# Performance work log

Measured on AMD Instinct MI355X. Metric: run time of the kernel, lower is better.

The kernel has to match this reference:

```python
import jax, jax.numpy as jnp
import numpy as np

N = 8192
IN_FEATS = 512
OUT_FEATS = 512


def setup_inputs() -> dict:
    key = jax.random.key(0)
    k_adj, k_feat, k_w = jax.random.split(key, 3)
    adj = jax.random.uniform(k_adj, (N, N), dtype=jnp.float32)
    features = jax.random.normal(k_feat, (N, IN_FEATS), dtype=jnp.float32)
    # nn.Linear(in_feats, out_feats, bias=False): weight is [out, in]; we store transposed [in, out]
    W = jax.random.normal(k_w, (IN_FEATS, OUT_FEATS), dtype=jnp.float32) / np.sqrt(IN_FEATS)
    return {"adj": adj, "features": features, "W": W}


def reference(adj, features, W):
    n = adj.shape[0]
    # adj + I (self loops)
    a = adj + jnp.eye(n, dtype=adj.dtype)
    # symmetric degree normalization D^{-1/2} A D^{-1/2}
    deg = jnp.sum(a, axis=1)  # [N]
    d_inv_sqrt = jnp.where(deg > 0, jax.lax.rsqrt(deg), 0.0)  # inf -> 0 as in torch code
    # diag(d) @ a @ diag(d) == d[:,None] * a * d[None,:] (algebraic simplification of O(N^3) diag matmuls)
    norm_adj = d_inv_sqrt[:, None] * a * d_inv_sqrt[None, :]  # [N, N]
    h = norm_adj @ features  # [N, in]
    return h @ W  # [N, out]
```

## Files before the change

### kernel.cpp

```cpp
#include <hip/hip_runtime.h>
#include <cstdint>
#include <cstddef>

#define NN 8192
#define NF 512
#define SPLITK 4

typedef __attribute__((ext_vector_type(8))) short bf16x8;
typedef __attribute__((ext_vector_type(8))) unsigned short u16x8;
typedef __attribute__((ext_vector_type(4))) float f32x4;

__device__ __forceinline__ unsigned short f2bf_bits(float f) {
  unsigned u = __builtin_bit_cast(unsigned, f);
  u += 0x7FFFu + ((u >> 16) & 1u);
  return (unsigned short)(u >> 16);
}

__device__ __forceinline__ float bf2f(unsigned short b) {
  return __builtin_bit_cast(float, (unsigned)b << 16);
}

__device__ __forceinline__ bf16x8 cvt8(float4 a, float4 b) {
  bf16x8 r;
  r[0] = (short)f2bf_bits(a.x); r[1] = (short)f2bf_bits(a.y);
  r[2] = (short)f2bf_bits(a.z); r[3] = (short)f2bf_bits(a.w);
  r[4] = (short)f2bf_bits(b.x); r[5] = (short)f2bf_bits(b.y);
  r[6] = (short)f2bf_bits(b.z); r[7] = (short)f2bf_bits(b.w);
  return r;
}

__device__ __forceinline__ void gld_lds16(const void* g, void* l) {
  __builtin_amdgcn_global_load_lds(
      (const __attribute__((address_space(1))) unsigned int*)g,
      (__attribute__((address_space(3))) unsigned int*)l, 16, 0, 0);
}

template <bool CVT>
__global__ void k_rowsum(const float* __restrict__ adj, float* __restrict__ dinv,
                         short* __restrict__ adjb) {
  const int row = blockIdx.x;
  const float4* p = (const float4*)(adj + (size_t)row * NN);
  short* ob = CVT ? (adjb + (size_t)row * NN) : nullptr;
  float s = 0.f;
#pragma unroll
  for (int j = 0; j < 8; ++j) {
    float4 v = p[j * 256 + threadIdx.x];
    s += (v.x + v.y) + (v.z + v.w);
    if (CVT) {
      ushort4 o;
      o.x = f2bf_bits(v.x); o.y = f2bf_bits(v.y);
      o.z = f2bf_bits(v.z); o.w = f2bf_bits(v.w);
      *(ushort4*)&ob[(size_t)(j * 256 + threadIdx.x) * 4] = o;
    }
  }
#pragma unroll
  for (int off = 32; off > 0; off >>= 1) s += __shfl_down(s, off, 64);
  __shared__ float red[4];
  if ((threadIdx.x & 63) == 0) red[threadIdx.x >> 6] = s;
  __syncthreads();
  if (threadIdx.x == 0) {
    float deg = red[0] + red[1] + red[2] + red[3] + 1.0f;
    dinv[row] = (deg > 0.f) ? (1.0f / sqrtf(deg)) : 0.f;
  }
}

__global__ void k_transpose2(const float* __restrict__ feat, const float* __restrict__ W,
                             const float* __restrict__ dinv,
                             short* __restrict__ FbT, short* __restrict__ WbT) {
  __shared__ float tile[32][33];
  const bool isF = (blockIdx.y < (NN / 32));
  const float* src = isF ? feat : W;
  short* dst = isF ? FbT : WbT;
  const int rows = isF ? NN : NF;
  const int r0 = (isF ? blockIdx.y : (blockIdx.y - NN / 32)) * 32;
  const int c0 = blockIdx.x * 32;
  const int tx = threadIdx.x & 31, ty = threadIdx.x >> 5;
#pragma unroll
  for (int i = 0; i < 32; i += 8) {
    float v = src[(size_t)(r0 + ty + i) * NF + c0 + tx];
    if (isF) v *= dinv[r0 + ty + i];
    tile[ty + i][tx] = v;
  }
  __syncthreads();
#pragma unroll
  for (int i = 0; i < 32; i += 8)
    dst[(size_t)(c0 + ty + i) * rows + r0 + tx] = (short)f2bf_bits(tile[tx][ty + i]);
}

__global__ __launch_bounds__(512, 1)
void k_gemm8(const short* __restrict__ Ab, const short* __restrict__ Bt,
             int N, int K, unsigned short* __restrict__ Pout) {
  __shared__ __align__(16) short As[3][2][256 * 32];
  __shared__ __align__(16) short Bs[2][2][256 * 32];
  const int tid = threadIdx.x, lane = tid & 63, w = tid >> 6;
  const int wm = w >> 2, wn = w & 3;

  const int hid = (blockIdx.z * gridDim.y + blockIdx.y) * gridDim.x + blockIdx.x;
  const int xcd = hid & 7, rr = hid >> 3;
  const int pair = xcd * 16 + (rr >> 1);
  const int member = rr & 1;
  const int m0 = (pair & 31) * 256;
  const int n0 = member * 256;
  const int kz = pair >> 5;
  const int ksl = K / SPLITK;
  const int kbase = kz * ksl;
  const int nt = ksl >> 6;
  unsigned short* Cp = Pout + (size_t)kz * ((size_t)NN * (size_t)N);

  f32x4 acc[8][4];
#pragma unroll
  for (int m = 0; m < 8; ++m)
#pragma unroll
    for (int n = 0; n < 4; ++n) acc[m][n] = (f32x4){0.f, 0.f, 0.f, 0.f};

  const int lr = lane & 15, kg = lane >> 4;

  auto stageA = [&](int buf, int t) {
#pragma unroll
    for (int h = 0; h < 2; ++h) {
      const int kofs = kbase + (t << 6) + (h << 5) + ((lane & 3) << 3);
#pragma unroll
      for (int rnd = 0; rnd < 2; ++rnd) {
        const int rowb = (rnd << 7) + (w << 4);
        const int row = rowb + (lane >> 2);
        gld_lds16(Ab + (size_t)(m0 + row) * K + kofs, &As[buf][h][rowb << 5]);
      }
    }
  };
  auto stageB = [&](int buf, int t) {
#pragma unroll
    for (int h = 0; h < 2; ++h) {
      const int kofs = kbase + (t << 6) + (h << 5) + ((lane & 3) << 3);
#pragma unroll
      for (int rnd = 0; rnd < 2; ++rnd) {
        const int rowb = (rnd << 7) + (w << 4);
        const int row = rowb + (lane >> 2);
        gld_lds16(Bt + (size_t)(n0 + row) * K + kofs, &Bs[buf][h][rowb << 5]);
      }
    }
  };
  auto readA = [&](int buf, int kh, bf16x8* a) {
#pragma unroll
    for (int mf = 0; mf < 8; ++mf)
      a[mf] = *(const bf16x8*)&As[buf][kh][(((wm << 7) + (mf << 4) + lr) << 5) + (kg << 3)];
  };
  auto readB2 = [&](int buf, int kh, int nh, bf16x8* b) {
#pragma unroll
    for (int i = 0; i < 2; ++i)
      b[i] = *(const bf16x8*)&Bs[buf][kh][(((wn << 6) + (((nh << 1) + i) << 4) + lr) << 5) + (kg << 3)];
  };
  auto mfma16 = [&](bf16x8* a, bf16x8* b, int nh) {
#pragma unroll
    for (int mf = 0; mf < 8; ++mf)
#pragma unroll
      for (int i = 0; i < 2; ++i)
        acc[mf][(nh << 1) + i] =
            __builtin_amdgcn_mfma_f32_16x16x32_bf16(a[mf], b[i], acc[mf][(nh << 1) + i], 0, 0, 0);
  };

  stageA(0, 0);
  stageB(0, 0);
  stageA(1, 1);

  for (int t = 0; t < nt; ++t) {
    const int ab = t % 3, bb = t & 1;
    bf16x8 a[8], b0[2], b1[2];
    if (t + 1 < nt) asm volatile("s_waitcnt vmcnt(4)" ::: "memory");
    else            asm volatile("s_waitcnt vmcnt(0)" ::: "memory");
    __builtin_amdgcn_s_barrier();
    __builtin_amdgcn_sched_barrier(0);
    readA(ab, 0, a);
    readB2(bb, 0, 0, b0);
    if (t + 1 < nt) stageB((t + 1) & 1, t + 1);
    asm volatile("s_waitcnt lgkmcnt(0)" ::: "memory");
    __builtin_amdgcn_sched_barrier(0);
    __builtin_amdgcn_s_setprio(1);
    mfma16(a, b0, 0);
    __builtin_amdgcn_s_setprio(0);
    __builtin_amdgcn_sched_barrier(0);
    readB2(bb, 0, 1, b1);
    asm volatile("s_waitcnt lgkmcnt(0)" ::: "memory");
    __builtin_amdgcn_sched_barrier(0);
    __builtin_amdgcn_s_setprio(1);
    mfma16(a, b1, 1);
    __builtin_amdgcn_s_setprio(0);
    __builtin_amdgcn_sched_barrier(0);
    readA(ab, 1, a);
    readB2(bb, 1, 0, b0);
    if (t + 2 < nt) stageA((t + 2) % 3, t + 2);
    asm volatile("s_waitcnt lgkmcnt(0)" ::: "memory");
    __builtin_amdgcn_sched_barrier(0);
    __builtin_amdgcn_s_setprio(1);
    mfma16(a, b0, 0);
    __builtin_amdgcn_s_setprio(0);
    __builtin_amdgcn_sched_barrier(0);
    readB2(bb, 1, 1, b1);
    asm volatile("s_waitcnt lgkmcnt(0)" ::: "memory");
    __builtin_amdgcn_sched_barrier(0);
    __builtin_amdgcn_s_setprio(1);
    mfma16(a, b1, 1);
    __builtin_amdgcn_s_setprio(0);
    __builtin_amdgcn_sched_barrier(0);
  }

  const int cl = lane & 15, rg = lane >> 4;
#pragma unroll
  for (int mf = 0; mf < 8; ++mf)
#pragma unroll
    for (int nf = 0; nf < 4; ++nf)
#pragma unroll
      for (int j = 0; j < 4; ++j) {
        const int gi = m0 + (wm << 7) + (mf << 4) + (rg << 2) + j;
        const int gn = n0 + (wn << 6) + (nf << 4) + cl;
        Cp[(size_t)gi * N + gn] = f2bf_bits(acc[mf][nf][j]);
      }
}

__global__ void k_reduce(const unsigned short* __restrict__ P, const float* __restrict__ dinv,
                         const float* __restrict__ feat, short* __restrict__ Hb) {
  const size_t idx = ((size_t)blockIdx.x * 256 + threadIdx.x) * 8;
  const int i = (int)(idx >> 9);
  const size_t stride = (size_t)NN * NF;
  float s[8] = {0.f, 0.f, 0.f, 0.f, 0.f, 0.f, 0.f, 0.f};
#pragma unroll
  for (int kz = 0; kz < SPLITK; ++kz) {
    u16x8 v = *(const u16x8*)&P[kz * stride + idx];
#pragma unroll
    for (int j = 0; j < 8; ++j) s[j] += bf2f(v[j]);
  }
  const float d = dinv[i], d2 = d * d;
  float4 f0 = *(const float4*)&feat[idx];
  float4 f1 = *(const float4*)&feat[idx + 4];
  u16x8 o;
  o[0] = f2bf_bits(d * s[0] + d2 * f0.x);
  o[1] = f2bf_bits(d * s[1] + d2 * f0.y);
  o[2] = f2bf_bits(d * s[2] + d2 * f0.z);
  o[3] = f2bf_bits(d * s[3] + d2 * f0.w);
  o[4] = f2bf_bits(d * s[4] + d2 * f1.x);
  o[5] = f2bf_bits(d * s[5] + d2 * f1.y);
  o[6] = f2bf_bits(d * s[6] + d2 * f1.z);
  o[7] = f2bf_bits(d * s[7] + d2 * f1.w);
  *(u16x8*)&Hb[idx] = o;
}

template <bool A_BF16, bool GCN_EPI>
__global__ __launch_bounds__(512, 2)
void k_gemm2(const void* __restrict__ Ap, const short* __restrict__ Bt,
             int N, int K,
             const float* __restrict__ dinv, const float* __restrict__ feat,
             void* __restrict__ Cp) {
  __shared__ __align__(16) short As[4][128 * 64];
  __shared__ __align__(16) short Bs[4][128 * 64];
  const int tid = threadIdx.x;
  const int lane = tid & 63;
  const int w = tid >> 6;
  const int wm = (w >> 1) & 1, wn = w & 1, kk = w >> 2;

  const int bid = blockIdx.y * gridDim.x + blockIdx.x;
  const int nb = gridDim.x * gridDim.y;
  const int sbid = ((nb & 7) == 0) ? ((bid & 7) * (nb >> 3) + (bid >> 3)) : bid;
  const int n0 = (sbid % gridDim.x) * 128;
  const int m0 = (sbid / gridDim.x) * 128;
  const int nt = K >> 6;

  f32x4 acc[4][4];
#pragma unroll
  for (int m = 0; m < 4; ++m)
#pragma unroll
    for (int n = 0; n < 4; ++n) acc[m][n] = (f32x4){0.f, 0.f, 0.f, 0.f};

  const int lr = lane & 15, kg = lane >> 4;
  const int lc = (kk << 2) + kg;

  auto stage_b = [&](int buf, int t) {
    const int kofs = t << 6;
#pragma unroll
    for (int q = 0; q < 2; ++q) {
      const int rblk = (w << 4) + (q << 3);
      const int r = rblk + (lane >> 3);
      const int sc = (lane & 7) ^ (r & 7);
      gld_lds16(Bt + (size_t)(n0 + r) * K + kofs + (sc << 3), &Bs[buf][rblk << 6]);
    }
  };
  auto stage_a = [&](int buf, int t) {
    const int kofs = t << 6;
    const short* Ab = (const short*)Ap;
#pragma unroll
    for (int q = 0; q < 2; ++q) {
      const int rblk = (w << 4) + (q << 3);
      const int r = rblk + (lane >> 3);
      const int sc = (lane & 7) ^ (r & 7);
      gld_lds16(Ab + (size_t)(m0 + r) * K + kofs + (sc << 3), &As[buf][rblk << 6]);
    }
  };
  auto stage_a_f32 = [&](int buf, int t) {
    const int kofs = t << 6;
    const float* Af = (const float*)Ap;
    const int r = tid >> 2;
    const int c0 = (tid & 3) << 4;
    const float* s = Af + (size_t)(m0 + r) * K + kofs + c0;
    float4 x0 = ((const float4*)s)[0], x1 = ((const float4*)s)[1];
    float4 x2 = ((const float4*)s)[2], x3 = ((const float4*)s)[3];
    const int cc = (tid & 3) << 1;
    *(bf16x8*)&As[buf][(r << 6) + ((cc ^ (r & 7)) << 3)]       = cvt8(x0, x1);
    *(bf16x8*)&As[buf][(r << 6) + (((cc + 1) ^ (r & 7)) << 3)] = cvt8(x2, x3);
  };
  auto read_a = [&](int buf, bf16x8* a) {
#pragma unroll
    for (int m = 0; m < 4; ++m) {
      const int r = (wm << 6) + (m << 4) + lr;
      a[m] = *(const bf16x8*)&As[buf][(r << 6) + ((lc ^ (r & 7)) << 3)];
    }
  };
  auto read_b2 = [&](int buf, int nh, bf16x8* b) {
#pragma unroll
    for (int i = 0; i < 2; ++i) {
      const int r = (wn << 6) + (((nh << 1) + i) << 4) + lr;
      b[i] = *(const bf16x8*)&Bs[buf][(r << 6) + ((lc ^ (r & 7)) << 3)];
    }
  };
  auto mfma8 = [&](bf16x8* a, bf16x8* b, int nh) {
#pragma unroll
    for (int m = 0; m < 4; ++m)
#pragma unroll
      for (int i = 0; i < 2; ++i)
        acc[m][(nh << 1) + i] =
            __builtin_amdgcn_mfma_f32_16x16x32_bf16(a[m], b[i], acc[m][(nh << 1) + i], 0, 0, 0);
  };

  if constexpr (A_BF16) {
    stage_a(0, 0); stage_b(0, 0);
    stage_a(1, 1); stage_b(1, 1);
    asm volatile("s_waitcnt vmcnt(4)" ::: "memory");
    __builtin_amdgcn_s_barrier();
    __builtin_amdgcn_sched_barrier(0);
    for (int t = 0; t < nt; ++t) {
      const int cur = t & 3;
      const bool more = (t + 2 < nt);
      bf16x8 a[4], b0[2], b1[2];
      read_a(cur, a);
      read_b2(cur, 0, b0);
      if (more) stage_a((t + 2) & 3, t + 2);
      __builtin_amdgcn_s_barrier();
      asm volatile("s_waitcnt lgkmcnt(0)" ::: "memory");
      __builtin_amdgcn_sched_barrier(0);
      __builtin_amdgcn_s_setprio(1);
      mfma8(a, b0, 0);
      __builtin_amdgcn_s_setprio(0);
      __builtin_amdgcn_sched_barrier(0);
      read_b2(cur, 1, b1);
      if (more) stage_b((t + 2) & 3, t + 2);
      asm volatile("s_waitcnt lgkmcnt(0)" ::: "memory");
      __builtin_amdgcn_sched_barrier(0);
      __builtin_amdgcn_s_setprio(1);
      mfma8(a, b1, 1);
      __builtin_amdgcn_s_setprio(0);
      __builtin_amdgcn_sched_barrier(0);
      if (more)            asm volatile("s_waitcnt vmcnt(4)" ::: "memory");
      else if (t + 1 < nt) asm volatile("s_waitcnt vmcnt(0)" ::: "memory");
      __builtin_amdgcn_s_barrier();
      __builtin_amdgcn_sched_barrier(0);
    }
  } else {
    stage_a_f32(0, 0); stage_b(0, 0);
    stage_a_f32(1, 1); stage_b(1, 1);
    __syncthreads();
    for (int t = 0; t < nt; ++t) {
      const int cur = t & 3;
      if (t + 2 < nt) { stage_a_f32((t + 2) & 3, t + 2); stage_b((t + 2) & 3, t + 2); }
      bf16x8 a[4], b0[2], b1[2];
      read_a(cur, a); read_b2(cur, 0, b0); read_b2(cur, 1, b1);
      __builtin_amdgcn_s_setprio(1);
      mfma8(a, b0, 0); mfma8(a, b1, 1);
      __builtin_amdgcn_s_setprio(0);
      __syncthreads();
    }
  }

  __syncthreads();
  float* red = (float*)&As[0][0];
  if (w >= 4) {
    float* my = red + ((w - 4) << 12);
#pragma unroll
    for (int m = 0; m < 4; ++m)
#pragma unroll
      for (int n = 0; n < 4; ++n)
        *(f32x4*)&my[(((m << 2) + n) << 8) + (lane << 2)] = acc[m][n];
  }
  __syncthreads();
  if (w < 4) {
    float* my = red + (w << 12);
#pragma unroll
    for (int m = 0; m < 4; ++m)
#pragma unroll
      for (int n = 0; n < 4; ++n)
        acc[m][n] += *(const f32x4*)&my[(((m << 2) + n) << 8) + (lane << 2)];
    const int cl = lane & 15, rg = lane >> 4;
#pragma unroll
    for (int m = 0; m < 4; ++m)
#pragma unroll
      for (int n = 0; n < 4; ++n)
#pragma unroll
        for (int j = 0; j < 4; ++j) {
          const int gi = m0 + (wm << 6) + (m << 4) + (rg << 2) + j;
          const int gn = n0 + (wn << 6) + (n << 4) + cl;
          const float v = acc[m][n][j];
          if constexpr (GCN_EPI) {
            const float d = dinv[gi];
            const float hv = d * v + d * d * feat[(size_t)gi * NF + gn];
            ((unsigned short*)Cp)[(size_t)gi * N + gn] = f2bf_bits(hv);
          } else {
            ((float*)Cp)[(size_t)gi * N + gn] = v;
          }
        }
  }
}

extern "C" void kernel_launch(void* const* d_in, const int* in_sizes, int n_in,
                              void* d_out, int out_size, void* d_ws, size_t ws_size,
                              hipStream_t stream) {
  const float* adj  = (const float*)d_in[0];
  const float* feat = (const float*)d_in[1];
  const float* W    = (const float*)d_in[2];

  char* ws = (char*)d_ws;
  float* dinv = (float*)ws;
  short* FbT  = (short*)(ws + 32768);
  short* WbT  = (short*)(ws + 32768 + 8388608);
  short* Hb   = (short*)(ws + 32768 + 8388608 + 524288);
  short* adjb = (short*)(ws + 32768 + 8388608 + 524288 + 8388608);
  unsigned short* part = (unsigned short*)(ws + 32768 + 8388608 + 524288 + 8388608 + 134217728);
  float* out  = (float*)d_out;
  const size_t need = (size_t)32768 + 8388608 + 524288 + 8388608 + 134217728 +
                      (size_t)SPLITK * NN * NF * 2;
  const bool big_ws = ws_size >= need;

  if (big_ws) {
    k_rowsum<true><<<NN, 256, 0, stream>>>(adj, dinv, adjb);
  } else {
    k_rowsum<false><<<NN, 256, 0, stream>>>(adj, dinv, nullptr);
  }
  k_transpose2<<<dim3(NF / 32, NN / 32 + NF / 32), 256, 0, stream>>>(feat, W, dinv, FbT, WbT);

  if (big_ws) {
    k_gemm8<<<dim3(NF / 256, NN / 256, SPLITK), 512, 0, stream>>>(adjb, FbT, NF, NN, part);
    k_reduce<<<(NN * NF) / (256 * 8), 256, 0, stream>>>(part, dinv, feat, Hb);
  } else {
    k_gemm2<false, true><<<dim3(NF / 128, NN / 128), 512, 0, stream>>>(
        adj, FbT, NF, NN, dinv, feat, Hb);
  }
  k_gemm2<true, false><<<dim3(NF / 128, NN / 128), 512, 0, stream>>>(
      Hb, WbT, NF, NF, nullptr, nullptr, out);
}
```

Before: 171.5 us.

## Switch main GEMM to 32x32x16 MFMA with XOR-swizzled LDS layout

The main split-K GEMM kernel now uses 32x32x16 bf16 MFMA instructions instead of 16x16x32, with 16-wide accumulators per fragment. The fragment read pattern changes to match. An XOR swizzle on the 16-byte k-blocks of LDS staging rows is added to avoid bank conflicts under the new access pattern. This aims for fewer MFMA issues and fewer LDS reads per unit of math. In exchange, the epilogue store mapping changes and register pressure goes up.

```diff
diff --git a/kernel.cpp b/kernel.cpp
--- a/kernel.cpp
+++ b/kernel.cpp
@@ -9,6 +9,7 @@
 typedef __attribute__((ext_vector_type(8))) short bf16x8;
 typedef __attribute__((ext_vector_type(8))) unsigned short u16x8;
 typedef __attribute__((ext_vector_type(4))) float f32x4;
+typedef __attribute__((ext_vector_type(16))) float f32x16;
 
 __device__ __forceinline__ unsigned short f2bf_bits(float f) {
   unsigned u = __builtin_bit_cast(unsigned, f);
@@ -107,22 +108,25 @@
   const int nt = ksl >> 6;
   unsigned short* Cp = Pout + (size_t)kz * ((size_t)NN * (size_t)N);
 
-  f32x4 acc[8][4];
-#pragma unroll
-  for (int m = 0; m < 8; ++m)
-#pragma unroll
-    for (int n = 0; n < 4; ++n) acc[m][n] = (f32x4){0.f, 0.f, 0.f, 0.f};
-
-  const int lr = lane & 15, kg = lane >> 4;
+  f32x16 acc[4][2];
+#pragma unroll
+  for (int m = 0; m < 4; ++m)
+#pragma unroll
+    for (int n = 0; n < 2; ++n)
+#pragma unroll
+      for (int r = 0; r < 16; ++r) acc[m][n][r] = 0.f;
+
+  const int l31 = lane & 31, hi = lane >> 5;
 
   auto stageA = [&](int buf, int t) {
 #pragma unroll
     for (int h = 0; h < 2; ++h) {
-      const int kofs = kbase + (t << 6) + (h << 5) + ((lane & 3) << 3);
 #pragma unroll
       for (int rnd = 0; rnd < 2; ++rnd) {
         const int rowb = (rnd << 7) + (w << 4);
         const int row = rowb + (lane >> 2);
+        const int blk = (lane & 3) ^ (row & 3);
+        const int kofs = kbase + (t << 6) + (h << 5) + (blk << 3);
         gld_lds16(Ab + (size_t)(m0 + row) * K + kofs, &As[buf][h][rowb << 5]);
       }
     }
@@ -130,32 +134,41 @@
   auto stageB = [&](int buf, int t) {
 #pragma unroll
     for (int h = 0; h < 2; ++h) {
-      const int kofs = kbase + (t << 6) + (h << 5) + ((lane & 3) << 3);
 #pragma unroll
       for (int rnd = 0; rnd < 2; ++rnd) {
         const int rowb = (rnd << 7) + (w << 4);
         const int row = rowb + (lane >> 2);
+        const int blk = (lane & 3) ^ (row & 3);
+        const int kofs = kbase + (t << 6) + (h << 5) + (blk << 3);
         gld_lds16(Bt + (size_t)(n0 + row) * K + kofs, &Bs[buf][h][rowb << 5]);
       }
     }
   };
-  auto readA = [&](int buf, int kh, bf16x8* a) {
-#pragma unroll
-    for (int mf = 0; mf < 8; ++mf)
-      a[mf] = *(const bf16x8*)&As[buf][kh][(((wm << 7) + (mf << 4) + lr) << 5) + (kg << 3)];
-  };
-  auto readB2 = [&](int buf, int kh, int nh, bf16x8* b) {
-#pragma unroll
-    for (int i = 0; i < 2; ++i)
-      b[i] = *(const bf16x8*)&Bs[buf][kh][(((wn << 6) + (((nh << 1) + i) << 4) + lr) << 5) + (kg << 3)];
-  };
-  auto mfma16 = [&](bf16x8* a, bf16x8* b, int nh) {
-#pragma unroll
-    for (int mf = 0; mf < 8; ++mf)
-#pragma unroll
-      for (int i = 0; i < 2; ++i)
-        acc[mf][(nh << 1) + i] =
-            __builtin_amdgcn_mfma_f32_16x16x32_bf16(a[mf], b[i], acc[mf][(nh << 1) + i], 0, 0, 0);
+  auto readA = [&](int buf, int h, bf16x8* a) {
+#pragma unroll
+    for (int mf = 0; mf < 4; ++mf)
+#pragma unroll
+      for (int ks = 0; ks < 2; ++ks) {
+        const int row = (wm << 7) + (mf << 5) + l31;
+        const int blk = ((ks << 1) + hi) ^ (row & 3);
+        a[(mf << 1) + ks] = *(const bf16x8*)&As[buf][h][(row << 5) + (blk << 3)];
+      }
+  };
+  auto readB = [&](int buf, int h, int nf, bf16x8* b) {
+#pragma unroll
+    for (int ks = 0; ks < 2; ++ks) {
+      const int row = (wn << 6) + (nf << 5) + l31;
+      const int blk = ((ks << 1) + hi) ^ (row & 3);
+      b[ks] = *(const bf16x8*)&Bs[buf][h][(row << 5) + (blk << 3)];
+    }
+  };
+  auto mfma8 = [&](bf16x8* a, bf16x8* b, int nf) {
+#pragma unroll
+    for (int mf = 0; mf < 4; ++mf)
+#pragma unroll
+      for (int ks = 0; ks < 2; ++ks)
+        acc[mf][nf] = __builtin_amdgcn_mfma_f32_32x32x16_bf16(
+            a[(mf << 1) + ks], b[ks], acc[mf][nf], 0, 0, 0);
   };
 
   stageA(0, 0);
@@ -170,49 +183,49 @@
     __builtin_amdgcn_s_barrier();
     __builtin_amdgcn_sched_barrier(0);
     readA(ab, 0, a);
-    readB2(bb, 0, 0, b0);
+    readB(bb, 0, 0, b0);
     if (t + 1 < nt) stageB((t + 1) & 1, t + 1);
     asm volatile("s_waitcnt lgkmcnt(0)" ::: "memory");
     __builtin_amdgcn_sched_barrier(0);
     __builtin_amdgcn_s_setprio(1);
-    mfma16(a, b0, 0);
+    mfma8(a, b0, 0);
     __builtin_amdgcn_s_setprio(0);
     __builtin_amdgcn_sched_barrier(0);
-    readB2(bb, 0, 1, b1);
+    readB(bb, 0, 1, b1);
     asm volatile("s_waitcnt lgkmcnt(0)" ::: "memory");
     __builtin_amdgcn_sched_barrier(0);
     __builtin_amdgcn_s_setprio(1);
-    mfma16(a, b1, 1);
+    mfma8(a, b1, 1);
     __builtin_amdgcn_s_setprio(0);
     __builtin_amdgcn_sched_barrier(0);
     readA(ab, 1, a);
-    readB2(bb, 1, 0, b0);
+    readB(bb, 1, 0, b0);
     if (t + 2 < nt) stageA((t + 2) % 3, t + 2);
     asm volatile("s_waitcnt lgkmcnt(0)" ::: "memory");
     __builtin_amdgcn_sched_barrier(0);
     __builtin_amdgcn_s_setprio(1);
-    mfma16(a, b0, 0);
+    mfma8(a, b0, 0);
     __builtin_amdgcn_s_setprio(0);
     __builtin_amdgcn_sched_barrier(0);
-    readB2(bb, 1, 1, b1);
+    readB(bb, 1, 1, b1);
     asm volatile("s_waitcnt lgkmcnt(0)" ::: "memory");
     __builtin_amdgcn_sched_barrier(0);
     __builtin_amdgcn_s_setprio(1);
-    mfma16(a, b1, 1);
+    mfma8(a, b1, 1);
     __builtin_amdgcn_s_setprio(0);
     __builtin_amdgcn_sched_barrier(0);
   }
 
-  const int cl = lane & 15, rg = lane >> 4;
-#pragma unroll
-  for (int mf = 0; mf < 8; ++mf)
-#pragma unroll
-    for (int nf = 0; nf < 4; ++nf)
-#pragma unroll
-      for (int j = 0; j < 4; ++j) {
-        const int gi = m0 + (wm << 7) + (mf << 4) + (rg << 2) + j;
-        const int gn = n0 + (wn << 6) + (nf << 4) + cl;
-        Cp[(size_t)gi * N + gn] = f2bf_bits(acc[mf][nf][j]);
+#pragma unroll
+  for (int mf = 0; mf < 4; ++mf)
+#pragma unroll
+    for (int nf = 0; nf < 2; ++nf)
+#pragma unroll
+      for (int reg = 0; reg < 16; ++reg) {
+        const int rowf = (reg & 3) + ((reg >> 2) << 3) + (hi << 2);
+        const int gi = m0 + (wm << 7) + (mf << 5) + rowf;
+        const int gn = n0 + (wn << 6) + (nf << 5) + l31;
+        Cp[(size_t)gi * N + gn] = f2bf_bits(acc[mf][nf][reg]);
       }
 }
 
```

Result: slower. 178.6 us (+4.1%).

## Fuse split-K reduction and GCN normalization into second GEMM A-staging

Applied to the files above, without the earlier changes.

Removes the separate reduce kernel and instead sums the split-K bf16 partials, applies the degree scaling and self-loop term, and converts to bf16 while staging A tiles of the H@W GEMM. This removes one launch and the Hb intermediate write/read. In exchange, each partial tile and feature row is re-read by every column block of the second GEMM, and that GEMM now uses the simpler synchronous staging path instead of the tuned async bf16 pipeline.

```diff
diff --git a/kernel.cpp b/kernel.cpp
--- a/kernel.cpp
+++ b/kernel.cpp
@@ -216,34 +216,7 @@
       }
 }
 
-__global__ void k_reduce(const unsigned short* __restrict__ P, const float* __restrict__ dinv,
-                         const float* __restrict__ feat, short* __restrict__ Hb) {
-  const size_t idx = ((size_t)blockIdx.x * 256 + threadIdx.x) * 8;
-  const int i = (int)(idx >> 9);
-  const size_t stride = (size_t)NN * NF;
-  float s[8] = {0.f, 0.f, 0.f, 0.f, 0.f, 0.f, 0.f, 0.f};
-#pragma unroll
-  for (int kz = 0; kz < SPLITK; ++kz) {
-    u16x8 v = *(const u16x8*)&P[kz * stride + idx];
-#pragma unroll
-    for (int j = 0; j < 8; ++j) s[j] += bf2f(v[j]);
-  }
-  const float d = dinv[i], d2 = d * d;
-  float4 f0 = *(const float4*)&feat[idx];
-  float4 f1 = *(const float4*)&feat[idx + 4];
-  u16x8 o;
-  o[0] = f2bf_bits(d * s[0] + d2 * f0.x);
-  o[1] = f2bf_bits(d * s[1] + d2 * f0.y);
-  o[2] = f2bf_bits(d * s[2] + d2 * f0.z);
-  o[3] = f2bf_bits(d * s[3] + d2 * f0.w);
-  o[4] = f2bf_bits(d * s[4] + d2 * f1.x);
-  o[5] = f2bf_bits(d * s[5] + d2 * f1.y);
-  o[6] = f2bf_bits(d * s[6] + d2 * f1.z);
-  o[7] = f2bf_bits(d * s[7] + d2 * f1.w);
-  *(u16x8*)&Hb[idx] = o;
-}
-
-template <bool A_BF16, bool GCN_EPI>
+template <int MODE>
 __global__ __launch_bounds__(512, 2)
 void k_gemm2(const void* __restrict__ Ap, const short* __restrict__ Bt,
              int N, int K,
@@ -305,6 +278,34 @@
     *(bf16x8*)&As[buf][(r << 6) + ((cc ^ (r & 7)) << 3)]       = cvt8(x0, x1);
     *(bf16x8*)&As[buf][(r << 6) + (((cc + 1) ^ (r & 7)) << 3)] = cvt8(x2, x3);
   };
+  auto stage_a_fused = [&](int buf, int t) {
+    const int kofs = t << 6;
+    const unsigned short* Pp = (const unsigned short*)Ap;
+    const int r = tid >> 2;
+    const int c0 = (tid & 3) << 4;
+    const int gi = m0 + r;
+    const size_t base = (size_t)gi * K + kofs + c0;
+    const size_t str = (size_t)NN * NF;
+    float s[16];
+#pragma unroll
+    for (int j = 0; j < 16; ++j) s[j] = 0.f;
+#pragma unroll
+    for (int kz = 0; kz < SPLITK; ++kz) {
+      u16x8 v0 = *(const u16x8*)&Pp[kz * str + base];
+      u16x8 v1 = *(const u16x8*)&Pp[kz * str + base + 8];
+#pragma unroll
+      for (int j = 0; j < 8; ++j) { s[j] += bf2f(v0[j]); s[8 + j] += bf2f(v1[j]); }
+    }
+    const float d = dinv[gi], d2 = d * d;
+    float h[16];
+#pragma unroll
+    for (int j = 0; j < 16; ++j) h[j] = d * s[j] + d2 * feat[base + j];
+    float4 h0 = {h[0], h[1], h[2], h[3]},   h1 = {h[4], h[5], h[6], h[7]};
+    float4 h2 = {h[8], h[9], h[10], h[11]}, h3 = {h[12], h[13], h[14], h[15]};
+    const int cc = (tid & 3) << 1;
+    *(bf16x8*)&As[buf][(r << 6) + ((cc ^ (r & 7)) << 3)]       = cvt8(h0, h1);
+    *(bf16x8*)&As[buf][(r << 6) + (((cc + 1) ^ (r & 7)) << 3)] = cvt8(h2, h3);
+  };
   auto read_a = [&](int buf, bf16x8* a) {
 #pragma unroll
     for (int m = 0; m < 4; ++m) {
@@ -328,7 +329,7 @@
             __builtin_amdgcn_mfma_f32_16x16x32_bf16(a[m], b[i], acc[m][(nh << 1) + i], 0, 0, 0);
   };
 
-  if constexpr (A_BF16) {
+  if constexpr (MODE == 0) {
     stage_a(0, 0); stage_b(0, 0);
     stage_a(1, 1); stage_b(1, 1);
     asm volatile("s_waitcnt vmcnt(4)" ::: "memory");
@@ -362,12 +363,17 @@
       __builtin_amdgcn_sched_barrier(0);
     }
   } else {
-    stage_a_f32(0, 0); stage_b(0, 0);
-    stage_a_f32(1, 1); stage_b(1, 1);
+    if constexpr (MODE == 1) { stage_a_f32(0, 0); stage_a_f32(1, 1); }
+    else                     { stage_a_fused(0, 0); stage_a_fused(1, 1); }
+    stage_b(0, 0); stage_b(1, 1);
     __syncthreads();
     for (int t = 0; t < nt; ++t) {
       const int cur = t & 3;
-      if (t + 2 < nt) { stage_a_f32((t + 2) & 3, t + 2); stage_b((t + 2) & 3, t + 2); }
+      if (t + 2 < nt) {
+        if constexpr (MODE == 1) stage_a_f32((t + 2) & 3, t + 2);
+        else                     stage_a_fused((t + 2) & 3, t + 2);
+        stage_b((t + 2) & 3, t + 2);
+      }
       bf16x8 a[4], b0[2], b1[2];
       read_a(cur, a); read_b2(cur, 0, b0); read_b2(cur, 1, b1);
       __builtin_amdgcn_s_setprio(1);
@@ -405,7 +411,7 @@
           const int gi = m0 + (wm << 6) + (m << 4) + (rg << 2) + j;
           const int gn = n0 + (wn << 6) + (n << 4) + cl;
           const float v = acc[m][n][j];
-          if constexpr (GCN_EPI) {
+          if constexpr (MODE == 1) {
             const float d = dinv[gi];
             const float hv = d * v + d * d * feat[(size_t)gi * NF + gn];
             ((unsigned short*)Cp)[(size_t)gi * N + gn] = f2bf_bits(hv);
@@ -444,11 +450,12 @@
 
   if (big_ws) {
     k_gemm8<<<dim3(NF / 256, NN / 256, SPLITK), 512, 0, stream>>>(adjb, FbT, NF, NN, part);
-    k_reduce<<<(NN * NF) / (256 * 8), 256, 0, stream>>>(part, dinv, feat, Hb);
+    k_gemm2<2><<<dim3(NF / 128, NN / 128), 512, 0, stream>>>(
+        part, WbT, NF, NF, dinv, feat, out);
   } else {
-    k_gemm2<false, true><<<dim3(NF / 128, NN / 128), 512, 0, stream>>>(
+    k_gemm2<1><<<dim3(NF / 128, NN / 128), 512, 0, stream>>>(
         adj, FbT, NF, NN, dinv, feat, Hb);
-  }
-  k_gemm2<true, false><<<dim3(NF / 128, NN / 128), 512, 0, stream>>>(
-      Hb, WbT, NF, NF, nullptr, nullptr, out);
-}
+    k_gemm2<0><<<dim3(NF / 128, NN / 128), 512, 0, stream>>>(
+        Hb, WbT, NF, NF, nullptr, nullptr, out);
+  }
+}
```

After: 172.3 us, median of 2. No clear change (+0.5%).
